# Performance work log

Hardware: AMD Instinct MI355X
Metric: run time of the kernel (lower is better)

The kernel has to match this reference:

```python
import jax, jax.numpy as jnp
import numpy as np

RADIUS = 3.0
BOX = 32.0
N = 8192


def setup_inputs() -> dict:
    key = jax.random.key(0)
    # atomic positions uniformly filling a [0, BOX]^3 box -> ~28 neighbors within RADIUS
    pos = jax.random.uniform(key, (N, 3), dtype=jnp.float32) * BOX
    return {"pos": pos}


def reference(pos):
    """radius_graph(pos, r=RADIUS, loop=True), returned as a dense [N, N] boolean
    adjacency mask (mask[i, j] = True iff ||pos_i - pos_j|| <= RADIUS).

    edge_index = nonzero(mask) is data-dependent in size, so the jit-friendly
    canonical output is the mask itself; loop=True means the diagonal is kept.
    """
    sq = jnp.sum(pos * pos, axis=-1)                      # [N]
    d2 = sq[:, None] + sq[None, :] - 2.0 * (pos @ pos.T)  # [N, N]
    d2 = jnp.maximum(d2, 0.0)                             # clamp fp error
    mask = d2 <= jnp.float32(RADIUS * RADIUS)             # loop=True: diag included
    return mask
```

## Files before the change

### kernel.cpp

```cpp
#include <hip/hip_runtime.h>


#define NPTS 8192
#define R2 9.0f

__global__ __launch_bounds__(256) void radius_mask_kernel(
    const float* __restrict__ pos, int* __restrict__ out) {
    const int i = blockIdx.y;
    const int j0 = (blockIdx.x * 256 + threadIdx.x) * 4;

    const float xi = pos[i * 3 + 0];
    const float yi = pos[i * 3 + 1];
    const float zi = pos[i * 3 + 2];
    const float sqi = __fadd_rn(__fadd_rn(__fmul_rn(xi, xi), __fmul_rn(yi, yi)),
                                __fmul_rn(zi, zi));

    const float4* p4 = reinterpret_cast<const float4*>(pos + (size_t)j0 * 3);
    const float4 a = p4[0];
    const float4 b = p4[1];
    const float4 c = p4[2];
    const float xj[4] = {a.x, a.w, b.z, c.y};
    const float yj[4] = {a.y, b.x, b.w, c.z};
    const float zj[4] = {a.z, b.y, c.x, c.w};

    int4 res;
    int* r = reinterpret_cast<int*>(&res);
#pragma unroll
    for (int k = 0; k < 4; ++k) {
        const float sqj = __fadd_rn(
            __fadd_rn(__fmul_rn(xj[k], xj[k]), __fmul_rn(yj[k], yj[k])),
            __fmul_rn(zj[k], zj[k]));
        const float dot = __fmaf_rn(zi, zj[k],
                           __fmaf_rn(yi, yj[k], __fmul_rn(xi, xj[k])));
        const float s = __fadd_rn(sqi, sqj);
        float d2 = __fsub_rn(s, __fmul_rn(2.0f, dot));
        d2 = fmaxf(d2, 0.0f);
        r[k] = (d2 <= R2) ? 1 : 0;
    }

    reinterpret_cast<int4*>(out)[((size_t)i * NPTS + j0) >> 2] = res;
}

extern "C" void kernel_launch(void* const* d_in, const int* in_sizes, int n_in,
                              void* d_out, int out_size, void* d_ws, size_t ws_size,
                              hipStream_t stream) {
    const float* pos = (const float*)d_in[0];
    int* out = (int*)d_out;

    dim3 grid(NPTS / (256 * 4), NPTS, 1);
    dim3 block(256, 1, 1);
    radius_mask_kernel<<<grid, block, 0, stream>>>(pos, out);
}
```

Measured before the change: 246.0 us.

## Precompute SoA positions and norms in prepass; use nontemporal output stores

Adds a small prepass kernel that converts positions to structure-of-arrays and precomputes squared norms into workspace. The main kernel then loads aligned float4 vectors per coordinate instead of recomputing norms, and writes the 256 MB int mask with nontemporal stores to avoid polluting cache. This adds an extra kernel launch and workspace dependency, but the main kernel is dominated by output write bandwidth.

```diff
diff --git a/kernel.cpp b/kernel.cpp
--- a/kernel.cpp
+++ b/kernel.cpp
@@ -4,41 +4,56 @@
 #define NPTS 8192
 #define R2 9.0f
 
+typedef int int4v __attribute__((ext_vector_type(4)));
+
+__global__ __launch_bounds__(256) void soa_kernel(
+    const float* __restrict__ pos, float* __restrict__ xs, float* __restrict__ ys,
+    float* __restrict__ zs, float* __restrict__ sq) {
+    const int j = blockIdx.x * 256 + threadIdx.x;
+    const float x = pos[j * 3 + 0];
+    const float y = pos[j * 3 + 1];
+    const float z = pos[j * 3 + 2];
+    xs[j] = x;
+    ys[j] = y;
+    zs[j] = z;
+    sq[j] = __fadd_rn(__fadd_rn(__fmul_rn(x, x), __fmul_rn(y, y)),
+                      __fmul_rn(z, z));
+}
+
 __global__ __launch_bounds__(256) void radius_mask_kernel(
-    const float* __restrict__ pos, int* __restrict__ out) {
+    const float* __restrict__ xs, const float* __restrict__ ys,
+    const float* __restrict__ zs, const float* __restrict__ sq,
+    int* __restrict__ out) {
     const int i = blockIdx.y;
     const int j0 = (blockIdx.x * 256 + threadIdx.x) * 4;
 
-    const float xi = pos[i * 3 + 0];
-    const float yi = pos[i * 3 + 1];
-    const float zi = pos[i * 3 + 2];
-    const float sqi = __fadd_rn(__fadd_rn(__fmul_rn(xi, xi), __fmul_rn(yi, yi)),
-                                __fmul_rn(zi, zi));
+    const float xi = xs[i];
+    const float yi = ys[i];
+    const float zi = zs[i];
+    const float sqi = sq[i];
 
-    const float4* p4 = reinterpret_cast<const float4*>(pos + (size_t)j0 * 3);
-    const float4 a = p4[0];
-    const float4 b = p4[1];
-    const float4 c = p4[2];
-    const float xj[4] = {a.x, a.w, b.z, c.y};
-    const float yj[4] = {a.y, b.x, b.w, c.z};
-    const float zj[4] = {a.z, b.y, c.x, c.w};
+    const float4 x4 = *reinterpret_cast<const float4*>(xs + j0);
+    const float4 y4 = *reinterpret_cast<const float4*>(ys + j0);
+    const float4 z4 = *reinterpret_cast<const float4*>(zs + j0);
+    const float4 q4 = *reinterpret_cast<const float4*>(sq + j0);
+    const float xj[4] = {x4.x, x4.y, x4.z, x4.w};
+    const float yj[4] = {y4.x, y4.y, y4.z, y4.w};
+    const float zj[4] = {z4.x, z4.y, z4.z, z4.w};
+    const float qj[4] = {q4.x, q4.y, q4.z, q4.w};
 
-    int4 res;
-    int* r = reinterpret_cast<int*>(&res);
+    int4v res;
 #pragma unroll
     for (int k = 0; k < 4; ++k) {
-        const float sqj = __fadd_rn(
-            __fadd_rn(__fmul_rn(xj[k], xj[k]), __fmul_rn(yj[k], yj[k])),
-            __fmul_rn(zj[k], zj[k]));
         const float dot = __fmaf_rn(zi, zj[k],
                            __fmaf_rn(yi, yj[k], __fmul_rn(xi, xj[k])));
-        const float s = __fadd_rn(sqi, sqj);
+        const float s = __fadd_rn(sqi, qj[k]);
         float d2 = __fsub_rn(s, __fmul_rn(2.0f, dot));
         d2 = fmaxf(d2, 0.0f);
-        r[k] = (d2 <= R2) ? 1 : 0;
+        res[k] = (d2 <= R2) ? 1 : 0;
     }
 
-    reinterpret_cast<int4*>(out)[((size_t)i * NPTS + j0) >> 2] = res;
+    __builtin_nontemporal_store(
+        res, reinterpret_cast<int4v*>(out) + (((size_t)i * NPTS + j0) >> 2));
 }
 
 extern "C" void kernel_launch(void* const* d_in, const int* in_sizes, int n_in,
@@ -47,7 +62,13 @@
     const float* pos = (const float*)d_in[0];
     int* out = (int*)d_out;
 
+    float* xs = (float*)d_ws;
+    float* ys = xs + NPTS;
+    float* zs = ys + NPTS;
+    float* sq = zs + NPTS;
+
+    soa_kernel<<<dim3(NPTS / 256), dim3(256), 0, stream>>>(pos, xs, ys, zs, sq);
+
     dim3 grid(NPTS / (256 * 4), NPTS, 1);
-    dim3 block(256, 1, 1);
-    radius_mask_kernel<<<grid, block, 0, stream>>>(pos, out);
+    radius_mask_kernel<<<grid, dim3(256), 0, stream>>>(xs, ys, zs, sq, out);
 }
```

Measured after the change: 257.9 us. 4.9% more time.
